# Performance work log

Hardware: AMD Instinct MI355X
Metric: run time of the kernel (lower is better)

Reference implementation:

```python
import jax, jax.numpy as jnp
import numpy as np

D_MODEL = 1024
N_HEADS = 16
HEAD_DIM = D_MODEL // N_HEADS


def setup_inputs() -> dict:
    key = jax.random.key(0)
    k_x, k_wqkv, k_bqkv, k_wo, k_bo = jax.random.split(key, 5)
    B, T = 2, 2048
    scale = 1.0 / np.sqrt(D_MODEL)
    return {
        "x": jax.random.normal(k_x, (B, T, D_MODEL), dtype=jnp.float32),
        "W_qkv": jax.random.normal(k_wqkv, (D_MODEL, 3 * D_MODEL), dtype=jnp.float32) * scale,
        "b_qkv": jax.random.normal(k_bqkv, (3 * D_MODEL,), dtype=jnp.float32) * 0.01,
        "W_out": jax.random.normal(k_wo, (D_MODEL, D_MODEL), dtype=jnp.float32) * scale,
        "b_out": jax.random.normal(k_bo, (D_MODEL,), dtype=jnp.float32) * 0.01,
    }


def reference(x, W_qkv, b_qkv, W_out, b_out):
    B, T, C = x.shape
    qkv = x @ W_qkv + b_qkv                      # [B,T,3C]
    q, k, v = jnp.split(qkv, 3, axis=-1)
    def heads(t):
        return t.reshape(B, T, N_HEADS, HEAD_DIM).transpose(0, 2, 1, 3)  # [B,H,T,d]
    q, k, v = heads(q), heads(k), heads(v)
    att = jnp.einsum('bhqd,bhkd->bhqk', q, k) / np.sqrt(HEAD_DIM)
    causal = jnp.tril(jnp.ones((T, T), dtype=bool))
    att = jnp.where(causal, att, -jnp.inf)
    att = jax.nn.softmax(att, axis=-1)
    out = jnp.einsum('bhqk,bhkd->bhqd', att, v)  # [B,H,T,d]
    out = out.transpose(0, 2, 1, 3).reshape(B, T, C)
    return out @ W_out + b_out
```

## Files before the change

### kernel.cpp

```cpp
#include <hip/hip_runtime.h>
#include <hip/hip_bf16.h>
#include <math.h>

typedef __bf16 bf16;
typedef __attribute__((ext_vector_type(8))) __bf16 bf16x8;
typedef __attribute__((ext_vector_type(4))) __bf16 bf16x4;
typedef __attribute__((ext_vector_type(4))) float f32x4;
typedef __attribute__((ext_vector_type(16))) float f32x16;
typedef __attribute__((ext_vector_type(4))) unsigned u32x4;

#define T_SEQ 2048

static __device__ __forceinline__ float fast_exp2(float x) {
#if __has_builtin(__builtin_amdgcn_exp2f)
    return __builtin_amdgcn_exp2f(x);
#else
    return __expf(x * 0.69314718f);
#endif
}

static __device__ __forceinline__ unsigned pk(float lo, float hi) {
    unsigned a = (unsigned)__builtin_bit_cast(unsigned short, (bf16)lo);
    unsigned b = (unsigned)__builtin_bit_cast(unsigned short, (bf16)hi);
    return a | (b << 16);
}

static __device__ __forceinline__ void gload_lds16(const bf16* g, bf16* l) {
    __builtin_amdgcn_global_load_lds((const __attribute__((address_space(1))) void*)g,
                                     (__attribute__((address_space(3))) void*)l, 16, 0, 0);
}

static __device__ __forceinline__ int swz(int row, int colb) {
    return row * 128 + (colb ^ ((row & 7) << 4));
}

__global__ __launch_bounds__(256) void prep_kernel(
    const float* __restrict__ x, bf16* __restrict__ xb,
    const float* __restrict__ W1, bf16* __restrict__ Wt1,
    const float* __restrict__ W2, bf16* __restrict__ Wt2)
{
    __shared__ float tile[32][33];
    const int bx = blockIdx.x, tid = threadIdx.x;
    if (bx < 2048) {
        const int n4 = (4096 * 1024) / 4;
        int i = bx * 256 + tid;
        const int stride = 2048 * 256;
        for (; i < n4; i += stride) {
            f32x4 v = ((const f32x4*)x)[i];
            bf16x4 o;
            o[0] = (bf16)v[0]; o[1] = (bf16)v[1]; o[2] = (bf16)v[2]; o[3] = (bf16)v[3];
            ((bf16x4*)xb)[i] = o;
        }
        return;
    }
    const float* W; bf16* Wt; int N, n0, k0;
    if (bx < 5120) {
        int idx = bx - 2048;
        W = W1; Wt = Wt1; N = 3072; n0 = (idx % 96) * 32; k0 = (idx / 96) * 32;
    } else {
        int idx = bx - 5120;
        W = W2; Wt = Wt2; N = 1024; n0 = (idx % 32) * 32; k0 = (idx / 32) * 32;
    }
    const int K = 1024;
    int tx = tid & 31, ty = tid >> 5;
#pragma unroll
    for (int j = 0; j < 4; ++j)
        tile[ty + j * 8][tx] = W[(size_t)(k0 + ty + j * 8) * N + n0 + tx];
    __syncthreads();
#pragma unroll
    for (int j = 0; j < 4; ++j)
        Wt[(size_t)(n0 + ty + j * 8) * K + k0 + tx] = (bf16)tile[tx][ty + j * 8];
}

template<int BM, int BN, int BLK, int WGN, int VMODE>
__global__ __launch_bounds__(BLK, 2) void gemm2ph_kernel(
    const bf16* __restrict__ A, const bf16* __restrict__ Bt,
    const float* __restrict__ bias, void* __restrict__ Cout,
    bf16* __restrict__ Vtout, int M, int N, int K, int GX)
{
    constexpr int WAVES = BLK / 64, WGM = WAVES / WGN;
    constexpr int MR = BM / (WGM * 16), NR = BN / (WGN * 16);
    constexpr int A_RND = BM * 8 / BLK, B_RND = BN * 8 / BLK;
    constexpr int LDS_HALF = (BM + BN) * 128;
    __shared__ __align__(16) char lds[2 * LDS_HALF];

    const int tid = threadIdx.x, lane = tid & 63, wid = tid >> 6;
    const int wm = wid / WGN, wn = wid % WGN;
    const int l15 = lane & 15, l4 = lane >> 4;
    const int cpx = gridDim.x >> 3;
    const int sbid = ((int)blockIdx.x & 7) * cpx + ((int)blockIdx.x >> 3);
    const int m0 = (sbid / GX) * BM, n0 = (sbid % GX) * BN;
    const int wu = tid & ~63;

    f32x4 acc[MR][NR] = {};
    const int NT = K >> 6;

    auto stage = [&](int b, int kt) {
        char* Ab = lds + b * LDS_HALF;
        char* Bb = Ab + BM * 128;
#pragma unroll
        for (int j = 0; j < A_RND; ++j) {
            int ch = j * BLK + tid, r = ch >> 3;
            int c = ((ch & 7) ^ (r & 7)) * 8;
            gload_lds16(&A[(size_t)(m0 + r) * K + kt + c],
                        (bf16*)Ab + (size_t)(j * BLK + wu) * 8);
        }
#pragma unroll
        for (int j = 0; j < B_RND; ++j) {
            int ch = j * BLK + tid, r = ch >> 3;
            int c = ((ch & 7) ^ (r & 7)) * 8;
            gload_lds16(&Bt[(size_t)(n0 + r) * K + kt + c],
                        (bf16*)Bb + (size_t)(j * BLK + wu) * 8);
        }
    };

    stage(0, 0);
    asm volatile("s_waitcnt vmcnt(0)" ::: "memory");
    __builtin_amdgcn_s_barrier();

    for (int t = 0; t < NT; ++t) {
        if (t + 1 < NT) stage((t + 1) & 1, (t + 1) * 64);
        const char* Ab = lds + (t & 1) * LDS_HALF;
        const char* Bb = Ab + BM * 128;
#pragma unroll
        for (int kk = 0; kk < 2; ++kk) {
            bf16x8 af[MR], bfr[NR];
#pragma unroll
            for (int mi = 0; mi < MR; ++mi) {
                int row = wm * (MR * 16) + mi * 16 + l15;
                af[mi] = *(const bf16x8*)(Ab + swz(row, kk * 64 + l4 * 16));
            }
#pragma unroll
            for (int ni = 0; ni < NR; ++ni) {
                int row = wn * (NR * 16) + ni * 16 + l15;
                bfr[ni] = *(const bf16x8*)(Bb + swz(row, kk * 64 + l4 * 16));
            }
#pragma unroll
            for (int mi = 0; mi < MR; ++mi)
#pragma unroll
                for (int ni = 0; ni < NR; ++ni)
                    acc[mi][ni] = __builtin_amdgcn_mfma_f32_16x16x32_bf16(
                        af[mi], bfr[ni], acc[mi][ni], 0, 0, 0);
        }
        asm volatile("s_waitcnt vmcnt(0)" ::: "memory");
        __builtin_amdgcn_s_barrier();
    }

#pragma unroll
    for (int ni = 0; ni < NR; ++ni) {
        const int colb = n0 + wn * (NR * 16) + ni * 16;
        const int col = colb + l15;
        float bv = bias[col];
        if (VMODE == 2 && colb >= 2048) {
            bf16* wtile = (bf16*)lds + wid * (16 * 72);
#pragma unroll
            for (int mi = 0; mi < MR; ++mi)
#pragma unroll
                for (int r = 0; r < 4; ++r)
                    wtile[l15 * 72 + mi * 16 + l4 * 4 + r] = (bf16)(acc[mi][ni][r] + bv);
            asm volatile("s_waitcnt lgkmcnt(0)" ::: "memory");
            const int hd_l = lane >> 2, tc = lane & 3;
            bf16x8 c0 = *(const bf16x8*)&wtile[hd_l * 72 + tc * 16];
            bf16x8 c1 = *(const bf16x8*)&wtile[hd_l * 72 + tc * 16 + 8];
            asm volatile("s_waitcnt lgkmcnt(0)" ::: "memory");
            const int row0 = m0 + wm * (MR * 16);
            const int bb = row0 >> 11, t0g = row0 & (T_SEQ - 1);
            bf16* dst = &Vtout[((size_t)(bb * 1024 + (colb - 2048) + hd_l)) * T_SEQ + t0g + tc * 16];
            *(bf16x8*)dst = c0;
            *(bf16x8*)(dst + 8) = c1;
        } else {
#pragma unroll
            for (int mi = 0; mi < MR; ++mi)
#pragma unroll
                for (int r = 0; r < 4; ++r) {
                    int row = m0 + wm * (MR * 16) + mi * 16 + l4 * 4 + r;
                    float v = acc[mi][ni][r] + bv;
                    if (VMODE) ((bf16*)Cout)[(size_t)row * N + col] = (bf16)v;
                    else       ((float*)Cout)[(size_t)row * N + col] = v;
                }
        }
    }
}

__global__ __launch_bounds__(256, 3) void attn_kernel(
    const bf16* __restrict__ qkv, const bf16* __restrict__ Vt, bf16* __restrict__ attb)
{
    __shared__ __align__(16) char smem[32768];
    const int tid = threadIdx.x, lane = tid & 63, wid = tid >> 6;
    const int qg = wid >> 1, par = wid & 1;
    const int bid = blockIdx.x;
    const int iq = 31 - (bid >> 5);
    const int bh = bid & 31, b = bh >> 4, h = bh & 15;
    const int nt = iq + 1, npairs = (nt + 1) >> 1;
    const int l31 = lane & 31, hi = lane >> 5, hib = hi * 16;
    const size_t base = (size_t)b * T_SEQ * 3072;
    const int koff = 1024 + h * 64;
    const size_t vtb = (size_t)bh * 64 * T_SEQ;
    const int sr = tid >> 2, sq4 = tid & 3;

    const int q0 = iq * 64 + qg * 32;
    const int qrow = q0 + l31;

    bf16x8 Qf[4];
#pragma unroll
    for (int ds = 0; ds < 4; ++ds)
        Qf[ds] = *(const bf16x8*)&qkv[base + (size_t)qrow * 3072 + h * 64 + ds * 16 + hi * 8];

    bf16x8 onesA;
#pragma unroll
    for (int j = 0; j < 8; ++j) onesA[j] = (bf16)1.0f;

    f32x16 Oacc[2] = {};
    f32x16 lacc = {};

    bf16x8 kreg[2][2], vreg[2][2];
    {
#pragma unroll
        for (int p = 0; p < 2; ++p)
#pragma unroll
            for (int j = 0; j < 2; ++j) {
                kreg[p][j] = *(const bf16x8*)&qkv[base + (size_t)(p * 64 + sr) * 3072
                                                 + koff + sq4 * 16 + j * 8];
                vreg[p][j] = *(const bf16x8*)&Vt[vtb + (size_t)sr * T_SEQ + p * 64 + sq4 * 16 + j * 8];
            }
    }

    for (int u = 0; u < npairs; ++u) {
        __syncthreads();
#pragma unroll
        for (int p = 0; p < 2; ++p) {
            char* Kp = smem + p * 8192;
            char* Vp = smem + 16384 + p * 8192;
#pragma unroll
            for (int j = 0; j < 2; ++j) {
                const int byte = swz(sr, sq4 * 32 + j * 16);
                *(bf16x8*)(Kp + byte) = kreg[p][j];
                *(bf16x8*)(Vp + byte) = vreg[p][j];
            }
        }
        __syncthreads();
        if (u + 1 < npairs) {
            const int pb = (u + 1) * 128;
#pragma unroll
            for (int p = 0; p < 2; ++p)
#pragma unroll
                for (int j = 0; j < 2; ++j) {
                    kreg[p][j] = *(const bf16x8*)&qkv[base + (size_t)(pb + p * 64 + sr) * 3072
                                                     + koff + sq4 * 16 + j * 8];
                    vreg[p][j] = *(const bf16x8*)&Vt[vtb + (size_t)sr * T_SEQ + pb + p * 64 + sq4 * 16 + j * 8];
                }
        }
        const int t = 2 * u + par;
        if (t < nt) {
            const char* Kc = smem + par * 8192;
            const char* Vc = smem + 16384 + par * 8192;
            f32x16 S[2] = {};
            __builtin_amdgcn_s_setprio(1);
#pragma unroll
            for (int ds = 0; ds < 4; ++ds)
#pragma unroll
                for (int kt = 0; kt < 2; ++kt) {
                    bf16x8 af = *(const bf16x8*)(Kc + swz(kt * 32 + l31, ds * 32 + hib));
                    S[kt] = __builtin_amdgcn_mfma_f32_32x32x16_bf16(af, Qf[ds], S[kt], 0, 0, 0);
                }
            __builtin_amdgcn_s_setprio(0);
            if (t == nt - 1) {
                const int qloc = qg * 32 + l31;
#pragma unroll
                for (int kt = 0; kt < 2; ++kt)
#pragma unroll
                    for (int j = 0; j < 16; ++j) {
                        const int kloc = kt * 32 + (j & 3) + 8 * (j >> 2) + 4 * hi;
                        if (kloc > qloc) S[kt][j] = -3.0e38f;
                    }
            }
#pragma unroll
            for (int kt = 0; kt < 2; ++kt)
#pragma unroll
                for (int j = 0; j < 16; ++j)
                    S[kt][j] = fast_exp2(S[kt][j] * 0.18033688f);
            __builtin_amdgcn_s_setprio(1);
#pragma unroll
            for (int ks = 0; ks < 4; ++ks) {
                const int kt = ks >> 1, bs = (ks & 1) * 8;
                unsigned P01 = pk(S[kt][bs + 0], S[kt][bs + 1]);
                unsigned P23 = pk(S[kt][bs + 2], S[kt][bs + 3]);
                unsigned P45 = pk(S[kt][bs + 4], S[kt][bs + 5]);
                unsigned P67 = pk(S[kt][bs + 6], S[kt][bs + 7]);
                auto r02 = __builtin_amdgcn_permlane32_swap(P01, P45, false, false);
                auto r13 = __builtin_amdgcn_permlane32_swap(P23, P67, false, false);
                u32x4 wv;
                wv[0] = r02[0]; wv[1] = r13[0]; wv[2] = r02[1]; wv[3] = r13[1];
                bf16x8 Bfrag = __builtin_bit_cast(bf16x8, wv);
#pragma unroll
                for (int dt = 0; dt < 2; ++dt) {
                    bf16x8 av = *(const bf16x8*)(Vc + swz(dt * 32 + l31, ks * 32 + hib));
                    Oacc[dt] = __builtin_amdgcn_mfma_f32_32x32x16_bf16(av, Bfrag, Oacc[dt], 0, 0, 0);
                }
                lacc = __builtin_amdgcn_mfma_f32_32x32x16_bf16(onesA, Bfrag, lacc, 0, 0, 0);
            }
            __builtin_amdgcn_s_setprio(0);
        }
    }

    float* cbuf = (float*)smem;
    __syncthreads();
    if (par == 1) {
        float* p = cbuf + (qg * 64 + lane) * 36;
#pragma unroll
        for (int dt = 0; dt < 2; ++dt)
#pragma unroll
            for (int j = 0; j < 16; ++j) p[dt * 16 + j] = Oacc[dt][j];
        p[32] = lacc[0];
    }
    __syncthreads();
    if (par == 0) {
        const float* p = cbuf + (qg * 64 + lane) * 36;
        float inv = 1.f / (lacc[0] + p[32]);
#pragma unroll
        for (int dt = 0; dt < 2; ++dt) {
#pragma unroll
            for (int g = 0; g < 4; ++g) {
                bf16x4 o;
#pragma unroll
                for (int j = 0; j < 4; ++j)
                    o[j] = (bf16)((Oacc[dt][g * 4 + j] + p[dt * 16 + g * 4 + j]) * inv);
                const int d = dt * 32 + g * 8 + 4 * hi;
                *(bf16x4*)&attb[((size_t)b * T_SEQ + qrow) * 1024 + h * 64 + d] = o;
            }
        }
    }
}

extern "C" void kernel_launch(void* const* d_in, const int* in_sizes, int n_in,
                              void* d_out, int out_size, void* d_ws, size_t ws_size,
                              hipStream_t stream)
{
    const float* x    = (const float*)d_in[0];
    const float* Wqkv = (const float*)d_in[1];
    const float* bqkv = (const float*)d_in[2];
    const float* Wout = (const float*)d_in[3];
    const float* bout = (const float*)d_in[4];
    float* out = (float*)d_out;

    char* ws = (char*)d_ws;
    bf16* xb    = (bf16*)(ws);
    bf16* Wqkvt = (bf16*)(ws + (8ull  << 20));
    bf16* Woutt = (bf16*)(ws + (14ull << 20));
    bf16* qkvb  = (bf16*)(ws + (16ull << 20));
    bf16* attb  = (bf16*)(ws + (40ull << 20));
    bf16* Vt    = (bf16*)(ws + (48ull << 20));

    prep_kernel<<<dim3(6144), dim3(256), 0, stream>>>(x, xb, Wqkv, Wqkvt, Wout, Woutt);
    gemm2ph_kernel<128, 192, 512, 4, 2><<<dim3(512), dim3(512), 0, stream>>>(
        xb, Wqkvt, bqkv, (void*)qkvb, Vt, 4096, 3072, 1024, 16);
    attn_kernel<<<dim3(1024), dim3(256), 0, stream>>>(qkvb, Vt, attb);
    gemm2ph_kernel<128, 64, 256, 2, 0><<<dim3(512), dim3(256), 0, stream>>>(
        attb, Woutt, bout, (void*)out, nullptr, 4096, 1024, 1024, 16);
}
```

Measured before the change: 86.47 us.

## Use 128-query attention blocks with 8 waves sharing each K/V tile load

The attention kernel now runs 512-thread blocks that each cover 128 query rows (four 32-row query groups times two key parities) instead of 64. Each K/V tile pair staged in shared memory is reused by twice as many query rows, which halves global K/V traffic per query, and each thread now loads one 64-row tile instead of two. Block order is interleaved between long and short causal rows to balance load, and the causal mask moves to global indices with a per-wave skip condition. The cost is more idle waves on diagonal tiles, a larger register budget per block, and fewer blocks (512) to spread across CUs.

```diff
diff --git a/kernel.cpp b/kernel.cpp
--- a/kernel.cpp
+++ b/kernel.cpp
@@ -182,23 +182,25 @@
     }
 }
 
-__global__ __launch_bounds__(256, 3) void attn_kernel(
+__global__ __launch_bounds__(512, 4) void attn_kernel(
     const bf16* __restrict__ qkv, const bf16* __restrict__ Vt, bf16* __restrict__ attb)
 {
-    __shared__ __align__(16) char smem[32768];
+    __shared__ __align__(16) char smem[36864];
     const int tid = threadIdx.x, lane = tid & 63, wid = tid >> 6;
     const int qg = wid >> 1, par = wid & 1;
     const int bid = blockIdx.x;
-    const int iq = 31 - (bid >> 5);
+    const int jb = bid >> 5;
+    const int iq = (jb < 8) ? (15 - 2 * jb) : (2 * (jb - 8));
     const int bh = bid & 31, b = bh >> 4, h = bh & 15;
-    const int nt = iq + 1, npairs = (nt + 1) >> 1;
+    const int npairs = iq + 1;
     const int l31 = lane & 31, hi = lane >> 5, hib = hi * 16;
     const size_t base = (size_t)b * T_SEQ * 3072;
     const int koff = 1024 + h * 64;
     const size_t vtb = (size_t)bh * 64 * T_SEQ;
-    const int sr = tid >> 2, sq4 = tid & 3;
-
-    const int q0 = iq * 64 + qg * 32;
+    const int sp = tid >> 8, st = tid & 255;
+    const int sr = st >> 2, sq4 = st & 3;
+
+    const int q0 = iq * 128 + qg * 32;
     const int qrow = q0 + l31;
 
     bf16x8 Qf[4];
@@ -213,45 +215,41 @@
     f32x16 Oacc[2] = {};
     f32x16 lacc = {};
 
-    bf16x8 kreg[2][2], vreg[2][2];
+    bf16x8 kreg[2], vreg[2];
     {
 #pragma unroll
-        for (int p = 0; p < 2; ++p)
-#pragma unroll
-            for (int j = 0; j < 2; ++j) {
-                kreg[p][j] = *(const bf16x8*)&qkv[base + (size_t)(p * 64 + sr) * 3072
-                                                 + koff + sq4 * 16 + j * 8];
-                vreg[p][j] = *(const bf16x8*)&Vt[vtb + (size_t)sr * T_SEQ + p * 64 + sq4 * 16 + j * 8];
-            }
+        for (int j = 0; j < 2; ++j) {
+            kreg[j] = *(const bf16x8*)&qkv[base + (size_t)(sp * 64 + sr) * 3072
+                                           + koff + sq4 * 16 + j * 8];
+            vreg[j] = *(const bf16x8*)&Vt[vtb + (size_t)sr * T_SEQ + sp * 64 + sq4 * 16 + j * 8];
+        }
     }
 
     for (int u = 0; u < npairs; ++u) {
         __syncthreads();
-#pragma unroll
-        for (int p = 0; p < 2; ++p) {
-            char* Kp = smem + p * 8192;
-            char* Vp = smem + 16384 + p * 8192;
+        {
+            char* Kp = smem + sp * 8192;
+            char* Vp = smem + 16384 + sp * 8192;
 #pragma unroll
             for (int j = 0; j < 2; ++j) {
                 const int byte = swz(sr, sq4 * 32 + j * 16);
-                *(bf16x8*)(Kp + byte) = kreg[p][j];
-                *(bf16x8*)(Vp + byte) = vreg[p][j];
+                *(bf16x8*)(Kp + byte) = kreg[j];
+                *(bf16x8*)(Vp + byte) = vreg[j];
             }
         }
         __syncthreads();
         if (u + 1 < npairs) {
             const int pb = (u + 1) * 128;
 #pragma unroll
-            for (int p = 0; p < 2; ++p)
-#pragma unroll
-                for (int j = 0; j < 2; ++j) {
-                    kreg[p][j] = *(const bf16x8*)&qkv[base + (size_t)(pb + p * 64 + sr) * 3072
-                                                     + koff + sq4 * 16 + j * 8];
-                    vreg[p][j] = *(const bf16x8*)&Vt[vtb + (size_t)sr * T_SEQ + pb + p * 64 + sq4 * 16 + j * 8];
-                }
+            for (int j = 0; j < 2; ++j) {
+                kreg[j] = *(const bf16x8*)&qkv[base + (size_t)(pb + sp * 64 + sr) * 3072
+                                               + koff + sq4 * 16 + j * 8];
+                vreg[j] = *(const bf16x8*)&Vt[vtb + (size_t)sr * T_SEQ + pb + sp * 64 + sq4 * 16 + j * 8];
+            }
         }
         const int t = 2 * u + par;
-        if (t < nt) {
+        const int k0g = t * 64;
+        if (k0g <= q0 + 31) {
             const char* Kc = smem + par * 8192;
             const char* Vc = smem + 16384 + par * 8192;
             f32x16 S[2] = {};
@@ -264,14 +262,13 @@
                     S[kt] = __builtin_amdgcn_mfma_f32_32x32x16_bf16(af, Qf[ds], S[kt], 0, 0, 0);
                 }
             __builtin_amdgcn_s_setprio(0);
-            if (t == nt - 1) {
-                const int qloc = qg * 32 + l31;
+            if (k0g + 63 > q0) {
 #pragma unroll
                 for (int kt = 0; kt < 2; ++kt)
 #pragma unroll
                     for (int j = 0; j < 16; ++j) {
-                        const int kloc = kt * 32 + (j & 3) + 8 * (j >> 2) + 4 * hi;
-                        if (kloc > qloc) S[kt][j] = -3.0e38f;
+                        const int kglob = k0g + kt * 32 + (j & 3) + 8 * (j >> 2) + 4 * hi;
+                        if (kglob > qrow) S[kt][j] = -3.0e38f;
                     }
             }
 #pragma unroll
@@ -354,7 +351,7 @@
     prep_kernel<<<dim3(6144), dim3(256), 0, stream>>>(x, xb, Wqkv, Wqkvt, Wout, Woutt);
     gemm2ph_kernel<128, 192, 512, 4, 2><<<dim3(512), dim3(512), 0, stream>>>(
         xb, Wqkvt, bqkv, (void*)qkvb, Vt, 4096, 3072, 1024, 16);
-    attn_kernel<<<dim3(1024), dim3(256), 0, stream>>>(qkvb, Vt, attb);
+    attn_kernel<<<dim3(512), dim3(512), 0, stream>>>(qkvb, Vt, attb);
     gemm2ph_kernel<128, 64, 256, 2, 0><<<dim3(512), dim3(256), 0, stream>>>(
         attb, Woutt, bout, (void*)out, nullptr, 4096, 1024, 1024, 16);
 }
```

After: 104.3 us. +20.6%, slower.
